# Optimization experiments

Hardware: AMD Instinct MI355X
Metric: run time of the kernel (lower is better)

## Reference

```python
import jax, jax.numpy as jnp
import numpy as np

D = 512    # feature_dim
NH = 8     # n_head
LQ = 1024  # query length
LK = 1024  # key/value length
B = 4      # batch
TEMP = 30.0


def setup_inputs() -> dict:
    key = jax.random.key(0)
    ks = jax.random.split(key, 10)
    s = (2.0 / D) ** 0.5  # init: normal(0, sqrt(2/out_features))
    t = lambda k, shp: jax.random.normal(k, shp, dtype=jnp.float32)
    return {
        'query_real': t(ks[0], (LQ, B, D)),
        'query_imag': t(ks[1], (LQ, B, D)),
        'key_real': t(ks[2], (LK, B, D)),
        'key_imag': t(ks[3], (LK, B, D)),
        'value_real': t(ks[4], (LK, B, D)),
        'value_imag': t(ks[5], (LK, B, D)),
        # per-head stacked Linear weights [NH, out, in] (torch Linear: x @ W.T + b)
        'WK_real': t(ks[6], (NH, D, D)) * s,
        'WK_imag': t(ks[7], (NH, D, D)) * s,
        'WV_real': t(ks[8], (NH, D, D)) * s,
        'WV_imag': t(ks[9], (NH, D, D)) * s,
        'bK_real': jnp.zeros((NH, D), jnp.float32),
        'bK_imag': jnp.zeros((NH, D), jnp.float32),
        'bV_real': jnp.zeros((NH, D), jnp.float32),
        'bV_imag': jnp.zeros((NH, D), jnp.float32),
    }


def reference(query_real, query_imag, key_real, key_imag, value_real, value_imag,
              WK_real, WK_imag, WV_real, WV_imag,
              bK_real, bK_imag, bV_real, bV_imag):
    # stacked per-head linear: x [L,B,D], W [H,E,D], b [H,E] -> [H,L,B,E]
    lin = lambda x, W, b: jnp.einsum('lbd,hed->hlbe', x, W) + b[:, None, None, :]
    # complex projection of keys with WK (real/imag parts)
    kr = lin(key_real, WK_real, bK_real) - lin(key_imag, WK_imag, bK_imag)
    ki = lin(key_real, WK_imag, bK_imag) + lin(key_imag, WK_real, bK_real)
    # queries are projected with the WV weights (as in the source)
    qr = lin(query_real, WV_real, bV_real) - lin(query_imag, WV_imag, bV_imag)
    qi = lin(query_real, WV_imag, bV_imag) + lin(query_imag, WV_real, bV_real)
    # complex dot product q*k (no conjugate), magnitude -> scores [H,B,Lq,Lk]
    dr = jnp.einsum('hqbd,hpbd->hbqp', qr, kr) - jnp.einsum('hqbd,hpbd->hbqp', qi, ki)
    di = jnp.einsum('hqbd,hpbd->hbqp', qi, kr) + jnp.einsum('hqbd,hpbd->hbqp', qr, ki)
    mag = jnp.sqrt(dr * dr + di * di)
    aff = jax.nn.softmax(mag * TEMP, axis=-1)  # softmax over keys
    # weighted value sum; values are the RAW inputs (not projected)
    out_real = jnp.einsum('hbqp,pbd->qbhd', aff, value_real).reshape(LQ, B, NH * D)
    out_imag = jnp.einsum('hbqp,pbd->qbhd', aff, value_imag).reshape(LQ, B, NH * D)
    return out_real, out_imag
```

## Files before the change

kernel.cpp:

```cpp
#include <hip/hip_runtime.h>
#include <math.h>

typedef _Float16 h8_t __attribute__((ext_vector_type(8)));
typedef _Float16 h4_t __attribute__((ext_vector_type(4)));
typedef float    f4_t __attribute__((ext_vector_type(4)));

#define MFMA16(a, b, c) __builtin_amdgcn_mfma_f32_16x16x32_f16((a), (b), (c), 0, 0, 0)

typedef const __attribute__((address_space(1))) void* gas1_t;
typedef __attribute__((address_space(3))) void* las3_t;
__device__ __forceinline__ void gload16(const void* g, void* l) {
  __builtin_amdgcn_global_load_lds((gas1_t)g, (las3_t)l, 16, 0, 0);
}

constexpr int L   = 1024;
constexpr int NB  = 4;
constexpr int NHh = 8;
constexpr int D   = 512;
constexpr int M1  = L * NB;
constexpr int K1  = 2 * D;
constexpr int N1  = NHh * 2 * D;
constexpr int HB  = NHh * NB;

constexpr size_t PL_A2 = (size_t)HB * L * K1 * 2;
constexpr size_t PL_BS = (size_t)HB * 3 * L * D * 2;
constexpr size_t OFF_R0 = 0;
constexpr size_t OFF_A2 = 134217728;
constexpr size_t OFF_BS = OFF_A2 + 2 * PL_A2;
constexpr size_t OFF_VT = OFF_BS + 2 * PL_BS;
constexpr size_t WS_NEED = OFF_VT + (size_t)NB * 1024 * 1024 * 2;
constexpr size_t PL_AX = (size_t)M1 * K1 * 2;
constexpr size_t ST_AQ = 0;
constexpr size_t ST_AK = 2 * PL_AX;
constexpr size_t PL_W  = (size_t)N1 * K1 * 2;
constexpr size_t ST_WQ = 4 * PL_AX;
constexpr size_t ST_WK = ST_WQ + 2 * PL_W;

static __device__ __forceinline__ void split32(float x, _Float16& hi, _Float16& lo) {
  _Float16 h = (_Float16)x;
  hi = h;
  lo = (_Float16)(x - (float)h);
}


__global__ void k_stage_x(const float* __restrict__ qre, const float* __restrict__ qim,
                          const float* __restrict__ kre, const float* __restrict__ kim,
                          _Float16* __restrict__ qhi, _Float16* __restrict__ qlo,
                          _Float16* __restrict__ khi, _Float16* __restrict__ klo) {
  const float* re; const float* im; _Float16* hi; _Float16* lo;
  if (blockIdx.y == 0) { re = qre; im = qim; hi = qhi; lo = qlo; }
  else                 { re = kre; im = kim; hi = khi; lo = klo; }
  int t = blockIdx.x * 256 + threadIdx.x;
  size_t idx = (size_t)t * 4;
  int m = (int)(idx >> 10), k = (int)(idx & 1023);
  const float* src = (k < 512) ? (re + (size_t)m * 512 + k) : (im + (size_t)m * 512 + (k - 512));
  f4_t v = *reinterpret_cast<const f4_t*>(src);
  h4_t h, l;
#pragma unroll
  for (int j = 0; j < 4; ++j) {
    _Float16 hh, ll; split32(v[j], hh, ll); h[j] = hh; l[j] = ll;
  }
  int sw = ((m >> 1) & 3) << 3;
  size_t dst = (size_t)m * 1024 + (k ^ sw);
  *reinterpret_cast<h4_t*>(hi + dst) = h;
  *reinterpret_cast<h4_t*>(lo + dst) = l;
}

__global__ void k_stage_w(const float* __restrict__ WVr, const float* __restrict__ WVi,
                          const float* __restrict__ WKr, const float* __restrict__ WKi,
                          _Float16* __restrict__ qhi, _Float16* __restrict__ qlo,
                          _Float16* __restrict__ khi, _Float16* __restrict__ klo) {
  const float* Wr; const float* Wi; _Float16* hi; _Float16* lo;
  if (blockIdx.y == 0) { Wr = WVr; Wi = WVi; hi = qhi; lo = qlo; }
  else                 { Wr = WKr; Wi = WKi; hi = khi; lo = klo; }
  int t = blockIdx.x * 256 + threadIdx.x;
  size_t idx = (size_t)t * 4;
  int n = (int)(idx >> 10), k = (int)(idx & 1023);
  int h = n >> 10, ri = (n >> 9) & 1, e = n & 511;
  size_t rowoff = ((size_t)(h * 512 + e)) * 512;
  const float* src; float sgn = 1.0f;
  if (ri == 0) {
    if (k < 512) src = Wr + rowoff + k;
    else { src = Wi + rowoff + (k - 512); sgn = -1.0f; }
  } else {
    if (k < 512) src = Wi + rowoff + k;
    else src = Wr + rowoff + (k - 512);
  }
  f4_t v = *reinterpret_cast<const f4_t*>(src);
  h4_t h4, l4;
#pragma unroll
  for (int j = 0; j < 4; ++j) {
    _Float16 hh, ll; split32(sgn * v[j], hh, ll); h4[j] = hh; l4[j] = ll;
  }
  int sw = ((n >> 1) & 3) << 3;
  size_t dst = (size_t)n * 1024 + (k ^ sw);
  *reinterpret_cast<h4_t*>(hi + dst) = h4;
  *reinterpret_cast<h4_t*>(lo + dst) = l4;
}

__global__ void k_stage_v(const float* __restrict__ vr, const float* __restrict__ vi,
                          _Float16* __restrict__ vt) {
  __shared__ float tile[64][65];
  int pt = blockIdx.x, nt = blockIdx.y, b = blockIdx.z;
  const float* src = (nt < 8) ? vr : vi;
  int dbase = (nt & 7) * 64;
  for (int i = threadIdx.x; i < 4096; i += 256) {
    int pl = i >> 6, dl = i & 63;
    tile[pl][dl] = src[((size_t)(pt * 64 + pl) * 4 + b) * 512 + dbase + dl];
  }
  __syncthreads();
  for (int i = threadIdx.x; i < 4096; i += 256) {
    int nl = i >> 6, pl = i & 63;
    int psw = pl ^ ((nl & 7) << 3);
    vt[((size_t)b * 1024 + nt * 64 + nl) * 1024 + pt * 64 + psw] = (_Float16)tile[pl][nl];
  }
}

__global__ __launch_bounds__(512, 1) void k_proj(
    const _Float16* __restrict__ Ahi, const _Float16* __restrict__ Alo,
    const _Float16* __restrict__ Bhi, const _Float16* __restrict__ Blo,
    const float* __restrict__ biasR, const float* __restrict__ biasI,
    _Float16* __restrict__ OutHi, _Float16* __restrict__ OutLo, int mode) {
  extern __shared__ __align__(16) _Float16 dldsP[];
  const int tid = threadIdx.x;
  const int id = blockIdx.x;
  const int xcd = id & 7, j = id >> 3;
  const int cm = j >> 2, cn = j & 3;
  const int m0 = cm * 256;
  const int n0 = (xcd * 4 + cn) * 256;
  const int wid = tid >> 6, lane = tid & 63;
  const int wm = (wid >> 1) * 64, wn = (wid & 1) * 128;
  const int fr = lane & 15, fq = lane >> 4;
  const int csw = (fq ^ ((fr >> 1) & 3)) * 8;

  const int srow = tid >> 2, sslot = tid & 3;
  const int soff = srow * 32 + sslot * 8;
  const _Float16* gA0 = Ahi + (size_t)(m0 + srow) * 1024 + sslot * 8;
  const _Float16* gA1 = gA0 + 128 * 1024;
  const _Float16* gA2 = Alo + (size_t)(m0 + srow) * 1024 + sslot * 8;
  const _Float16* gA3 = gA2 + 128 * 1024;
  const _Float16* gB0 = Bhi + (size_t)(n0 + srow) * 1024 + sslot * 8;
  const _Float16* gB1 = gB0 + 128 * 1024;
  const _Float16* gB2 = Blo + (size_t)(n0 + srow) * 1024 + sslot * 8;
  const _Float16* gB3 = gB2 + 128 * 1024;

  auto STAGE_A = [&](int buf) {
    _Float16* Lb = dldsP + buf * 32768;
    gload16(gA0, &Lb[soff]);
    gload16(gA1, &Lb[4096 + soff]);
    gload16(gA2, &Lb[8192 + soff]);
    gload16(gA3, &Lb[12288 + soff]);
    gA0 += 32; gA1 += 32; gA2 += 32; gA3 += 32;
  };
  auto STAGE_B = [&](int buf) {
    _Float16* Lb = dldsP + buf * 32768;
    gload16(gB0, &Lb[16384 + soff]);
    gload16(gB1, &Lb[20480 + soff]);
    gload16(gB2, &Lb[24576 + soff]);
    gload16(gB3, &Lb[28672 + soff]);
    gB0 += 32; gB1 += 32; gB2 += 32; gB3 += 32;
  };

  f4_t acc[4][8] = {};

  STAGE_A(0); STAGE_B(0);
  asm volatile("s_waitcnt vmcnt(0)" ::: "memory");
  __builtin_amdgcn_s_barrier();

  for (int kt = 0; kt < 32; ++kt) {
    const int cur = kt & 1, nxt = cur ^ 1;
    const _Float16* Lb = dldsP + cur * 32768;
    h8_t af[4][2];
#pragma unroll
    for (int mi = 0; mi < 4; ++mi) {
      int r = wm + mi * 16 + fr;
      af[mi][0] = *reinterpret_cast<const h8_t*>(&Lb[r * 32 + csw]);
      af[mi][1] = *reinterpret_cast<const h8_t*>(&Lb[8192 + r * 32 + csw]);
    }
    h8_t bh[4], bl[4];
#pragma unroll
    for (int ni = 0; ni < 4; ++ni) {
      int rn = wn + ni * 16 + fr;
      bh[ni] = *reinterpret_cast<const h8_t*>(&Lb[16384 + rn * 32 + csw]);
      bl[ni] = *reinterpret_cast<const h8_t*>(&Lb[24576 + rn * 32 + csw]);
    }
    if (kt < 31) STAGE_A(nxt);
    __builtin_amdgcn_s_barrier();
    __builtin_amdgcn_s_setprio(1);
#pragma unroll
    for (int ni = 0; ni < 4; ++ni)
#pragma unroll
      for (int mi = 0; mi < 4; ++mi) {
        acc[mi][ni] = MFMA16(af[mi][0], bh[ni], acc[mi][ni]);
        acc[mi][ni] = MFMA16(af[mi][0], bl[ni], acc[mi][ni]);
        acc[mi][ni] = MFMA16(af[mi][1], bh[ni], acc[mi][ni]);
      }
    __builtin_amdgcn_s_setprio(0);
    __builtin_amdgcn_s_barrier();
#pragma unroll
    for (int ni = 0; ni < 4; ++ni) {
      int rn = wn + (ni + 4) * 16 + fr;
      bh[ni] = *reinterpret_cast<const h8_t*>(&Lb[16384 + rn * 32 + csw]);
      bl[ni] = *reinterpret_cast<const h8_t*>(&Lb[24576 + rn * 32 + csw]);
    }
    if (kt < 31) STAGE_B(nxt);
    __builtin_amdgcn_s_barrier();
    __builtin_amdgcn_s_setprio(1);
#pragma unroll
    for (int ni = 0; ni < 4; ++ni)
#pragma unroll
      for (int mi = 0; mi < 4; ++mi) {
        acc[mi][ni + 4] = MFMA16(af[mi][0], bh[ni], acc[mi][ni + 4]);
        acc[mi][ni + 4] = MFMA16(af[mi][0], bl[ni], acc[mi][ni + 4]);
        acc[mi][ni + 4] = MFMA16(af[mi][1], bh[ni], acc[mi][ni + 4]);
      }
    __builtin_amdgcn_s_setprio(0);
    if (kt < 31) asm volatile("s_waitcnt vmcnt(0)" ::: "memory");
    __builtin_amdgcn_s_barrier();
  }

#pragma unroll
  for (int mi = 0; mi < 4; ++mi)
#pragma unroll
    for (int ni = 0; ni < 8; ++ni)
#pragma unroll
      for (int r = 0; r < 4; ++r) {
        int m = m0 + wm + mi * 16 + fq * 4 + r;
        int n = n0 + wn + ni * 16 + fr;
        int h = n >> 10, ri = (n >> 9) & 1, e = n & 511;
        float bias = (ri == 0) ? (biasR[h * 512 + e] - biasI[h * 512 + e])
                               : (biasI[h * 512 + e] + biasR[h * 512 + e]);
        float val = acc[mi][ni][r] + bias;
        _Float16 hi, lo; split32(val, hi, lo);
        int lb = m & 3;
        int lrow = m >> 2;
        int hb = h * 4 + lb;
        int sw = ((lrow >> 1) & 3) << 3;
        if (mode == 0) {
          size_t dst = ((size_t)hb * 1024 + lrow) * 1024 + ((ri * 512 + e) ^ sw);
          OutHi[dst] = hi; OutLo[dst] = lo;
        } else {
          int esw = e ^ sw;
          if (ri == 0) {
            size_t dst = (((size_t)hb * 3 + 0) * 1024 + lrow) * 512 + esw;
            OutHi[dst] = hi; OutLo[dst] = lo;
          } else {
            size_t d1 = (((size_t)hb * 3 + 1) * 1024 + lrow) * 512 + esw;
            size_t d2 = (((size_t)hb * 3 + 2) * 1024 + lrow) * 512 + esw;
            OutHi[d1] = hi;  OutLo[d1] = lo;
            OutHi[d2] = -hi; OutLo[d2] = -lo;
          }
        }
      }
}

__global__ __launch_bounds__(512, 1) void k_score(
    const _Float16* __restrict__ A2hi, const _Float16* __restrict__ A2lo,
    const _Float16* __restrict__ BShi, const _Float16* __restrict__ BSlo,
    float* __restrict__ mag) {
  extern __shared__ __align__(16) _Float16 dldsS[];
  const int tid = threadIdx.x;
  const int id = blockIdx.x;
  const int xcd = id & 7, j = id >> 3;
  const int hb = xcd * 4 + (j >> 5);
  const int r5 = j & 31;
  const int m0 = (r5 >> 3) * 256, n0 = (r5 & 7) * 128;
  const int wid = tid >> 6, lane = tid & 63;
  const int wm = (wid >> 1) * 64, wn = (wid & 1) * 64;
  const int fr = lane & 15, fq = lane >> 4;
  const int csw = (fq ^ ((fr >> 1) & 3)) * 8;

  const _Float16* Abh = A2hi + (size_t)hb * 1048576;
  const _Float16* Abl = A2lo + (size_t)hb * 1048576;
  const _Float16* BShb = BShi + (size_t)hb * 3 * 524288;
  const _Float16* BSlb = BSlo + (size_t)hb * 3 * 524288;

  const int srow = tid >> 2, sslot = tid & 3;
  const int soff = srow * 32 + sslot * 8;
  const size_t bbase = (size_t)(n0 + srow) * 512 + sslot * 8;
  const _Float16* gA0 = Abh + (size_t)(m0 + srow) * 1024 + sslot * 8;
  const _Float16* gA1 = gA0 + 128 * 1024;
  const _Float16* gA2 = Abl + (size_t)(m0 + srow) * 1024 + sslot * 8;
  const _Float16* gA3 = gA2 + 128 * 1024;
  const _Float16* gB0 = BShb + bbase;
  const _Float16* gB1 = BSlb + bbase;
  const _Float16* gB2 = BShb + 524288 + bbase;
  const _Float16* gB3 = BSlb + 524288 + bbase;

  auto STAGE_A = [&](int buf) {
    _Float16* Lb = dldsS + buf * 32768;
    gload16(gA0, &Lb[soff]);
    gload16(gA1, &Lb[4096 + soff]);
    gload16(gA2, &Lb[8192 + soff]);
    gload16(gA3, &Lb[12288 + soff]);
    gA0 += 32; gA1 += 32; gA2 += 32; gA3 += 32;
  };
  auto STAGE_B = [&](int buf, int kt) {
    if (kt == 16) {
      gB0 = BShb + 2 * 524288 + bbase;
      gB1 = BSlb + 2 * 524288 + bbase;
      gB2 = BShb + bbase;
      gB3 = BSlb + bbase;
    }
    _Float16* Lb = dldsS + buf * 32768;
    gload16(gB0, &Lb[16384 + soff]);
    gload16(gB1, &Lb[20480 + soff]);
    gload16(gB2, &Lb[24576 + soff]);
    gload16(gB3, &Lb[28672 + soff]);
    gB0 += 32; gB1 += 32; gB2 += 32; gB3 += 32;
  };

  f4_t adr[4][4] = {}, adi[4][4] = {};

  STAGE_A(0); STAGE_B(0, 0);
  asm volatile("s_waitcnt vmcnt(0)" ::: "memory");
  __builtin_amdgcn_s_barrier();

  for (int kt = 0; kt < 32; ++kt) {
    const int cur = kt & 1, nxt = cur ^ 1;
    const _Float16* Lb = dldsS + cur * 32768;
    h8_t af[4][2];
#pragma unroll
    for (int mi = 0; mi < 4; ++mi) {
      int r = wm + mi * 16 + fr;
      af[mi][0] = *reinterpret_cast<const h8_t*>(&Lb[r * 32 + csw]);
      af[mi][1] = *reinterpret_cast<const h8_t*>(&Lb[8192 + r * 32 + csw]);
    }
    h8_t drh[2], drl[2], dih[2], dil[2];
#pragma unroll
    for (int ni = 0; ni < 2; ++ni) {
      int rn = wn + ni * 16 + fr;
      drh[ni] = *reinterpret_cast<const h8_t*>(&Lb[16384 + rn * 32 + csw]);
      drl[ni] = *reinterpret_cast<const h8_t*>(&Lb[20480 + rn * 32 + csw]);
      dih[ni] = *reinterpret_cast<const h8_t*>(&Lb[24576 + rn * 32 + csw]);
      dil[ni] = *reinterpret_cast<const h8_t*>(&Lb[28672 + rn * 32 + csw]);
    }
    if (kt < 31) STAGE_A(nxt);
    __builtin_amdgcn_s_barrier();
    __builtin_amdgcn_s_setprio(1);
#pragma unroll
    for (int ni = 0; ni < 2; ++ni)
#pragma unroll
      for (int mi = 0; mi < 4; ++mi) {
        adr[mi][ni] = MFMA16(af[mi][0], drh[ni], adr[mi][ni]);
        adr[mi][ni] = MFMA16(af[mi][0], drl[ni], adr[mi][ni]);
        adr[mi][ni] = MFMA16(af[mi][1], drh[ni], adr[mi][ni]);
        adi[mi][ni] = MFMA16(af[mi][0], dih[ni], adi[mi][ni]);
        adi[mi][ni] = MFMA16(af[mi][0], dil[ni], adi[mi][ni]);
        adi[mi][ni] = MFMA16(af[mi][1], dih[ni], adi[mi][ni]);
      }
    __builtin_amdgcn_s_setprio(0);
    __builtin_amdgcn_s_barrier();
#pragma unroll
    for (int ni = 0; ni < 2; ++ni) {
      int rn = wn + (ni + 2) * 16 + fr;
      drh[ni] = *reinterpret_cast<const h8_t*>(&Lb[16384 + rn * 32 + csw]);
      drl[ni] = *reinterpret_cast<const h8_t*>(&Lb[20480 + rn * 32 + csw]);
      dih[ni] = *reinterpret_cast<const h8_t*>(&Lb[24576 + rn * 32 + csw]);
      dil[ni] = *reinterpret_cast<const h8_t*>(&Lb[28672 + rn * 32 + csw]);
    }
    if (kt < 31) STAGE_B(nxt, kt + 1);
    __builtin_amdgcn_s_barrier();
    __builtin_amdgcn_s_setprio(1);
#pragma unroll
    for (int ni = 0; ni < 2; ++ni)
#pragma unroll
      for (int mi = 0; mi < 4; ++mi) {
        adr[mi][ni + 2] = MFMA16(af[mi][0], drh[ni], adr[mi][ni + 2]);
        adr[mi][ni + 2] = MFMA16(af[mi][0], drl[ni], adr[mi][ni + 2]);
        adr[mi][ni + 2] = MFMA16(af[mi][1], drh[ni], adr[mi][ni + 2]);
        adi[mi][ni + 2] = MFMA16(af[mi][0], dih[ni], adi[mi][ni + 2]);
        adi[mi][ni + 2] = MFMA16(af[mi][0], dil[ni], adi[mi][ni + 2]);
        adi[mi][ni + 2] = MFMA16(af[mi][1], dih[ni], adi[mi][ni + 2]);
      }
    __builtin_amdgcn_s_setprio(0);
    if (kt < 31) asm volatile("s_waitcnt vmcnt(0)" ::: "memory");
    __builtin_amdgcn_s_barrier();
  }

  float* mb = mag + (size_t)hb * 1048576;
#pragma unroll
  for (int mi = 0; mi < 4; ++mi)
#pragma unroll
    for (int ni = 0; ni < 4; ++ni)
#pragma unroll
      for (int r = 0; r < 4; ++r) {
        int q = m0 + wm + mi * 16 + fq * 4 + r;
        int p = n0 + wn + ni * 16 + fr;
        float dr = adr[mi][ni][r], di = adi[mi][ni][r];
        mb[(size_t)q * 1024 + p] = sqrtf(dr * dr + di * di) * 30.0f;
      }
}

__global__ void k_softmax(const float* __restrict__ mag, _Float16* __restrict__ aff) {
  const size_t base = (size_t)blockIdx.x * 1024;
  const int q = blockIdx.x & 1023;
  const int sw = (q & 7) << 3;
  const int tid = threadIdx.x;
  const int wid = tid >> 6, lane = tid & 63;
  float v[4];
#pragma unroll
  for (int j = 0; j < 4; ++j) v[j] = mag[base + tid + j * 256];
  float mx = fmaxf(fmaxf(v[0], v[1]), fmaxf(v[2], v[3]));
#pragma unroll
  for (int o = 32; o > 0; o >>= 1) mx = fmaxf(mx, __shfl_xor(mx, o));
  __shared__ float red[8];
  if (lane == 0) red[wid] = mx;
  __syncthreads();
  mx = fmaxf(fmaxf(red[0], red[1]), fmaxf(red[2], red[3]));
  float e[4]; float s = 0.0f;
#pragma unroll
  for (int j = 0; j < 4; ++j) { e[j] = __expf(v[j] - mx); s += e[j]; }
#pragma unroll
  for (int o = 32; o > 0; o >>= 1) s += __shfl_xor(s, o);
  if (lane == 0) red[4 + wid] = s;
  __syncthreads();
  s = red[4] + red[5] + red[6] + red[7];
  float inv = 1.0f / s;
#pragma unroll
  for (int j = 0; j < 4; ++j) aff[base + j * 256 + (tid ^ sw)] = (_Float16)(e[j] * inv);
}

__global__ __launch_bounds__(256, 2) void k_pv(
    const _Float16* __restrict__ aff, const _Float16* __restrict__ vt,
    float* __restrict__ out) {
  extern __shared__ __align__(16) _Float16 dldsV[];
  const int tid = threadIdx.x;
  const int id = blockIdx.x;
  const int xcd = id & 7, j = id >> 3;
  const int b = xcd >> 1;
  const int h = (xcd & 1) * 4 + (j >> 6);
  const int hb = h * 4 + b;
  const int r6 = j & 63;
  const int m0 = (r6 >> 3) * 128, n0 = (r6 & 7) * 128;
  const int wid = tid >> 6, lane = tid & 63;
  const int wm = (wid >> 1) * 64, wn = (wid & 1) * 64;
  const int fr = lane & 15, fq = lane >> 4;
  const int s7 = fr & 7;

  const _Float16* Ab = aff + (size_t)hb * 1048576;
  const _Float16* Bb = vt + (size_t)b * 1048576;

  const int srow = tid >> 3, sslot = tid & 7;
  const int soff = srow * 64 + sslot * 8;
  const _Float16* gA = Ab + (size_t)(m0 + srow) * 1024 + sslot * 8;
  const _Float16* gB = Bb + (size_t)(n0 + srow) * 1024 + sslot * 8;

  auto STAGE = [&](int buf) {
    _Float16* Lb = dldsV + buf * 16384;
    gload16(gA,             &Lb[soff]);
    gload16(gA + 32 * 1024, &Lb[2048 + soff]);
    gload16(gA + 64 * 1024, &Lb[4096 + soff]);
    gload16(gA + 96 * 1024, &Lb[6144 + soff]);
    gload16(gB,             &Lb[8192 + soff]);
    gload16(gB + 32 * 1024, &Lb[10240 + soff]);
    gload16(gB + 64 * 1024, &Lb[12288 + soff]);
    gload16(gB + 96 * 1024, &Lb[14336 + soff]);
    gA += 64; gB += 64;
  };

  f4_t acc[4][4] = {};
  auto compute = [&](int buf) {
    const _Float16* Lb = dldsV + buf * 16384;
#pragma unroll
    for (int k32 = 0; k32 < 2; ++k32) {
      const int csw = ((k32 * 4 + fq) ^ s7) * 8;
      h8_t af[4];
#pragma unroll
      for (int mi = 0; mi < 4; ++mi)
        af[mi] = *reinterpret_cast<const h8_t*>(&Lb[(wm + mi * 16 + fr) * 64 + csw]);
#pragma unroll
      for (int ni = 0; ni < 4; ++ni) {
        h8_t bf = *reinterpret_cast<const h8_t*>(&Lb[8192 + (wn + ni * 16 + fr) * 64 + csw]);
#pragma unroll
        for (int mi = 0; mi < 4; ++mi) acc[mi][ni] = MFMA16(af[mi], bf, acc[mi][ni]);
      }
    }
  };

  STAGE(0);
  for (int kt = 0; kt < 15; ++kt) {
    __builtin_amdgcn_s_barrier();
    STAGE((kt + 1) & 1);
    asm volatile("s_waitcnt vmcnt(8)" ::: "memory");
    __builtin_amdgcn_s_barrier();
    compute(kt & 1);
  }
  __builtin_amdgcn_s_barrier();
  asm volatile("s_waitcnt vmcnt(0)" ::: "memory");
  __builtin_amdgcn_s_barrier();
  compute(1);

#pragma unroll
  for (int mi = 0; mi < 4; ++mi)
#pragma unroll
    for (int ni = 0; ni < 4; ++ni)
#pragma unroll
      for (int r = 0; r < 4; ++r) {
        int q = m0 + wm + mi * 16 + fq * 4 + r;
        int n = n0 + wn + ni * 16 + fr;
        int d = n & 511;
        size_t o = (size_t)(n < 512 ? 0 : 16777216) + (((size_t)q * 4 + b) * 8 + h) * 512 + d;
        out[o] = acc[mi][ni][r];
      }
}

extern "C" void kernel_launch(void* const* d_in, const int* in_sizes, int n_in,
                              void* d_out, int out_size, void* d_ws, size_t ws_size,
                              hipStream_t stream) {
  (void)in_sizes; (void)n_in; (void)out_size;
  if (ws_size < WS_NEED) return;

  hipFuncSetAttribute((const void*)k_score, hipFuncAttributeMaxDynamicSharedMemorySize, 131072);
  hipFuncSetAttribute((const void*)k_proj,  hipFuncAttributeMaxDynamicSharedMemorySize, 131072);
  hipFuncSetAttribute((const void*)k_pv,    hipFuncAttributeMaxDynamicSharedMemorySize, 65536);

  const float* qre = (const float*)d_in[0];
  const float* qim = (const float*)d_in[1];
  const float* kre = (const float*)d_in[2];
  const float* kim = (const float*)d_in[3];
  const float* vre = (const float*)d_in[4];
  const float* vim = (const float*)d_in[5];
  const float* WKr = (const float*)d_in[6];
  const float* WKi = (const float*)d_in[7];
  const float* WVr = (const float*)d_in[8];
  const float* WVi = (const float*)d_in[9];
  const float* bKr = (const float*)d_in[10];
  const float* bKi = (const float*)d_in[11];
  const float* bVr = (const float*)d_in[12];
  const float* bVi = (const float*)d_in[13];

  char* ws = (char*)d_ws;
  _Float16* AqHi = (_Float16*)(ws + ST_AQ);
  _Float16* AqLo = (_Float16*)(ws + ST_AQ + PL_AX);
  _Float16* AkHi = (_Float16*)(ws + ST_AK);
  _Float16* AkLo = (_Float16*)(ws + ST_AK + PL_AX);
  _Float16* WqHi = (_Float16*)(ws + ST_WQ);
  _Float16* WqLo = (_Float16*)(ws + ST_WQ + PL_W);
  _Float16* WkHi = (_Float16*)(ws + ST_WK);
  _Float16* WkLo = (_Float16*)(ws + ST_WK + PL_W);
  _Float16* A2Hi = (_Float16*)(ws + OFF_A2);
  _Float16* A2Lo = (_Float16*)(ws + OFF_A2 + PL_A2);
  _Float16* BSHi = (_Float16*)(ws + OFF_BS);
  _Float16* BSLo = (_Float16*)(ws + OFF_BS + PL_BS);
  _Float16* Vt   = (_Float16*)(ws + OFF_VT);
  float*    magp = (float*)(ws + OFF_R0);
  _Float16* affp = (_Float16*)(ws + OFF_A2);
  float*    outp = (float*)d_out;

  k_stage_x<<<dim3(4096, 2), dim3(256), 0, stream>>>(qre, qim, kre, kim, AqHi, AqLo, AkHi, AkLo);
  k_stage_w<<<dim3(8192, 2), dim3(256), 0, stream>>>(WVr, WVi, WKr, WKi, WqHi, WqLo, WkHi, WkLo);
  k_stage_v<<<dim3(16, 16, 4), dim3(256), 0, stream>>>(vre, vim, Vt);
  k_proj<<<dim3(512), dim3(512), 131072, stream>>>(AqHi, AqLo, WqHi, WqLo, bVr, bVi, A2Hi, A2Lo, 0);
  k_proj<<<dim3(512), dim3(512), 131072, stream>>>(AkHi, AkLo, WkHi, WkLo, bKr, bKi, BSHi, BSLo, 1);
  k_score<<<dim3(1024), dim3(512), 131072, stream>>>(A2Hi, A2Lo, BSHi, BSLo, magp);
  k_softmax<<<dim3(32 * 1024), dim3(256), 0, stream>>>(magp, affp);
  k_pv<<<dim3(2048), dim3(256), 65536, stream>>>(affp, Vt, outp);
}
```

Measured before the change: 907.8 us.

## Software-pipeline LDS fragment reads across k-steps in projection and score GEMMs

Restructures the main loops of both split-fp16 GEMM kernels so that next-tile LDS fragment reads (A and first B half) are issued ahead of the MFMA blocks of the current tile, merging A and B global-to-LDS staging into one issue. Barriers drop from four to two per k-step and sched_barrier fences keep the compiler from reordering MFMAs around the reads. This is meant to hide LDS read latency behind MFMAs and cut sync overhead, at the cost of extra fragment registers, which may lower occupancy.

```diff
diff --git a/kernel.cpp b/kernel.cpp
--- a/kernel.cpp
+++ b/kernel.cpp
@@ -6,6 +6,7 @@
 typedef float    f4_t __attribute__((ext_vector_type(4)));
 
 #define MFMA16(a, b, c) __builtin_amdgcn_mfma_f32_16x16x32_f16((a), (b), (c), 0, 0, 0)
+#define SCHEDB() __builtin_amdgcn_sched_barrier(0)
 
 typedef const __attribute__((address_space(1))) void* gas1_t;
 typedef __attribute__((address_space(3))) void* las3_t;
@@ -144,48 +145,60 @@
   const _Float16* gB2 = Blo + (size_t)(n0 + srow) * 1024 + sslot * 8;
   const _Float16* gB3 = gB2 + 128 * 1024;
 
-  auto STAGE_A = [&](int buf) {
+  auto STAGE = [&](int buf) {
     _Float16* Lb = dldsP + buf * 32768;
     gload16(gA0, &Lb[soff]);
     gload16(gA1, &Lb[4096 + soff]);
     gload16(gA2, &Lb[8192 + soff]);
     gload16(gA3, &Lb[12288 + soff]);
-    gA0 += 32; gA1 += 32; gA2 += 32; gA3 += 32;
-  };
-  auto STAGE_B = [&](int buf) {
-    _Float16* Lb = dldsP + buf * 32768;
     gload16(gB0, &Lb[16384 + soff]);
     gload16(gB1, &Lb[20480 + soff]);
     gload16(gB2, &Lb[24576 + soff]);
     gload16(gB3, &Lb[28672 + soff]);
+    gA0 += 32; gA1 += 32; gA2 += 32; gA3 += 32;
     gB0 += 32; gB1 += 32; gB2 += 32; gB3 += 32;
   };
 
   f4_t acc[4][8] = {};
-
-  STAGE_A(0); STAGE_B(0);
-  asm volatile("s_waitcnt vmcnt(0)" ::: "memory");
-  __builtin_amdgcn_s_barrier();
-
-  for (int kt = 0; kt < 32; ++kt) {
-    const int cur = kt & 1, nxt = cur ^ 1;
-    const _Float16* Lb = dldsP + cur * 32768;
-    h8_t af[4][2];
+  h8_t af[4][2], bh[4], bl[4], bh2[4], bl2[4];
+
+  auto READ_AF = [&](const _Float16* Lb) {
 #pragma unroll
     for (int mi = 0; mi < 4; ++mi) {
       int r = wm + mi * 16 + fr;
       af[mi][0] = *reinterpret_cast<const h8_t*>(&Lb[r * 32 + csw]);
       af[mi][1] = *reinterpret_cast<const h8_t*>(&Lb[8192 + r * 32 + csw]);
     }
-    h8_t bh[4], bl[4];
+  };
+  auto READ_B0 = [&](const _Float16* Lb) {
 #pragma unroll
     for (int ni = 0; ni < 4; ++ni) {
       int rn = wn + ni * 16 + fr;
       bh[ni] = *reinterpret_cast<const h8_t*>(&Lb[16384 + rn * 32 + csw]);
       bl[ni] = *reinterpret_cast<const h8_t*>(&Lb[24576 + rn * 32 + csw]);
     }
-    if (kt < 31) STAGE_A(nxt);
-    __builtin_amdgcn_s_barrier();
+  };
+  auto READ_B1 = [&](const _Float16* Lb) {
+#pragma unroll
+    for (int ni = 0; ni < 4; ++ni) {
+      int rn = wn + (ni + 4) * 16 + fr;
+      bh2[ni] = *reinterpret_cast<const h8_t*>(&Lb[16384 + rn * 32 + csw]);
+      bl2[ni] = *reinterpret_cast<const h8_t*>(&Lb[24576 + rn * 32 + csw]);
+    }
+  };
+
+  STAGE(0);
+  asm volatile("s_waitcnt vmcnt(0)" ::: "memory");
+  __builtin_amdgcn_s_barrier();
+  READ_AF(dldsP); READ_B0(dldsP);
+
+  for (int kt = 0; kt < 32; ++kt) {
+    const int cur = kt & 1, nxt = cur ^ 1;
+    const _Float16* Lc = dldsP + cur * 32768;
+    const _Float16* Ln = dldsP + nxt * 32768;
+    READ_B1(Lc);
+    if (kt < 31) STAGE(nxt);
+    SCHEDB();
     __builtin_amdgcn_s_setprio(1);
 #pragma unroll
     for (int ni = 0; ni < 4; ++ni)
@@ -196,26 +209,22 @@
         acc[mi][ni] = MFMA16(af[mi][1], bh[ni], acc[mi][ni]);
       }
     __builtin_amdgcn_s_setprio(0);
+    if (kt < 31) asm volatile("s_waitcnt vmcnt(0)" ::: "memory");
     __builtin_amdgcn_s_barrier();
-#pragma unroll
-    for (int ni = 0; ni < 4; ++ni) {
-      int rn = wn + (ni + 4) * 16 + fr;
-      bh[ni] = *reinterpret_cast<const h8_t*>(&Lb[16384 + rn * 32 + csw]);
-      bl[ni] = *reinterpret_cast<const h8_t*>(&Lb[24576 + rn * 32 + csw]);
-    }
-    if (kt < 31) STAGE_B(nxt);
-    __builtin_amdgcn_s_barrier();
+    if (kt < 31) READ_B0(Ln);
+    SCHEDB();
     __builtin_amdgcn_s_setprio(1);
 #pragma unroll
     for (int ni = 0; ni < 4; ++ni)
 #pragma unroll
       for (int mi = 0; mi < 4; ++mi) {
-        acc[mi][ni + 4] = MFMA16(af[mi][0], bh[ni], acc[mi][ni + 4]);
-        acc[mi][ni + 4] = MFMA16(af[mi][0], bl[ni], acc[mi][ni + 4]);
-        acc[mi][ni + 4] = MFMA16(af[mi][1], bh[ni], acc[mi][ni + 4]);
+        acc[mi][ni + 4] = MFMA16(af[mi][0], bh2[ni], acc[mi][ni + 4]);
+        acc[mi][ni + 4] = MFMA16(af[mi][0], bl2[ni], acc[mi][ni + 4]);
+        acc[mi][ni + 4] = MFMA16(af[mi][1], bh2[ni], acc[mi][ni + 4]);
       }
     __builtin_amdgcn_s_setprio(0);
-    if (kt < 31) asm volatile("s_waitcnt vmcnt(0)" ::: "memory");
+    SCHEDB();
+    if (kt < 31) READ_AF(Ln);
     __builtin_amdgcn_s_barrier();
   }
 
@@ -287,46 +296,40 @@
   const _Float16* gB2 = BShb + 524288 + bbase;
   const _Float16* gB3 = BSlb + 524288 + bbase;
 
-  auto STAGE_A = [&](int buf) {
+  auto STAGE = [&](int buf, int ktn) {
+    if (ktn == 16) {
+      gB0 = BShb + 2 * 524288 + bbase;
+      gB1 = BSlb + 2 * 524288 + bbase;
+      gB2 = BShb + bbase;
+      gB3 = BSlb + bbase;
+    }
     _Float16* Lb = dldsS + buf * 32768;
     gload16(gA0, &Lb[soff]);
     gload16(gA1, &Lb[4096 + soff]);
     gload16(gA2, &Lb[8192 + soff]);
     gload16(gA3, &Lb[12288 + soff]);
-    gA0 += 32; gA1 += 32; gA2 += 32; gA3 += 32;
-  };
-  auto STAGE_B = [&](int buf, int kt) {
-    if (kt == 16) {
-      gB0 = BShb + 2 * 524288 + bbase;
-      gB1 = BSlb + 2 * 524288 + bbase;
-      gB2 = BShb + bbase;
-      gB3 = BSlb + bbase;
-    }
-    _Float16* Lb = dldsS + buf * 32768;
     gload16(gB0, &Lb[16384 + soff]);
     gload16(gB1, &Lb[20480 + soff]);
     gload16(gB2, &Lb[24576 + soff]);
     gload16(gB3, &Lb[28672 + soff]);
+    gA0 += 32; gA1 += 32; gA2 += 32; gA3 += 32;
     gB0 += 32; gB1 += 32; gB2 += 32; gB3 += 32;
   };
 
   f4_t adr[4][4] = {}, adi[4][4] = {};
-
-  STAGE_A(0); STAGE_B(0, 0);
-  asm volatile("s_waitcnt vmcnt(0)" ::: "memory");
-  __builtin_amdgcn_s_barrier();
-
-  for (int kt = 0; kt < 32; ++kt) {
-    const int cur = kt & 1, nxt = cur ^ 1;
-    const _Float16* Lb = dldsS + cur * 32768;
-    h8_t af[4][2];
+  h8_t af[4][2];
+  h8_t drh[2], drl[2], dih[2], dil[2];
+  h8_t drh2[2], drl2[2], dih2[2], dil2[2];
+
+  auto READ_AF = [&](const _Float16* Lb) {
 #pragma unroll
     for (int mi = 0; mi < 4; ++mi) {
       int r = wm + mi * 16 + fr;
       af[mi][0] = *reinterpret_cast<const h8_t*>(&Lb[r * 32 + csw]);
       af[mi][1] = *reinterpret_cast<const h8_t*>(&Lb[8192 + r * 32 + csw]);
     }
-    h8_t drh[2], drl[2], dih[2], dil[2];
+  };
+  auto READ_B0 = [&](const _Float16* Lb) {
 #pragma unroll
     for (int ni = 0; ni < 2; ++ni) {
       int rn = wn + ni * 16 + fr;
@@ -335,8 +338,30 @@
       dih[ni] = *reinterpret_cast<const h8_t*>(&Lb[24576 + rn * 32 + csw]);
       dil[ni] = *reinterpret_cast<const h8_t*>(&Lb[28672 + rn * 32 + csw]);
     }
-    if (kt < 31) STAGE_A(nxt);
-    __builtin_amdgcn_s_barrier();
+  };
+  auto READ_B1 = [&](const _Float16* Lb) {
+#pragma unroll
+    for (int ni = 0; ni < 2; ++ni) {
+      int rn = wn + (ni + 2) * 16 + fr;
+      drh2[ni] = *reinterpret_cast<const h8_t*>(&Lb[16384 + rn * 32 + csw]);
+      drl2[ni] = *reinterpret_cast<const h8_t*>(&Lb[20480 + rn * 32 + csw]);
+      dih2[ni] = *reinterpret_cast<const h8_t*>(&Lb[24576 + rn * 32 + csw]);
+      dil2[ni] = *reinterpret_cast<const h8_t*>(&Lb[28672 + rn * 32 + csw]);
+    }
+  };
+
+  STAGE(0, 0);
+  asm volatile("s_waitcnt vmcnt(0)" ::: "memory");
+  __builtin_amdgcn_s_barrier();
+  READ_AF(dldsS); READ_B0(dldsS);
+
+  for (int kt = 0; kt < 32; ++kt) {
+    const int cur = kt & 1, nxt = cur ^ 1;
+    const _Float16* Lc = dldsS + cur * 32768;
+    const _Float16* Ln = dldsS + nxt * 32768;
+    READ_B1(Lc);
+    if (kt < 31) STAGE(nxt, kt + 1);
+    SCHEDB();
     __builtin_amdgcn_s_setprio(1);
 #pragma unroll
     for (int ni = 0; ni < 2; ++ni)
@@ -350,31 +375,25 @@
         adi[mi][ni] = MFMA16(af[mi][1], dih[ni], adi[mi][ni]);
       }
     __builtin_amdgcn_s_setprio(0);
+    if (kt < 31) asm volatile("s_waitcnt vmcnt(0)" ::: "memory");
     __builtin_amdgcn_s_barrier();
-#pragma unroll
-    for (int ni = 0; ni < 2; ++ni) {
-      int rn = wn + (ni + 2) * 16 + fr;
-      drh[ni] = *reinterpret_cast<const h8_t*>(&Lb[16384 + rn * 32 + csw]);
-      drl[ni] = *reinterpret_cast<const h8_t*>(&Lb[20480 + rn * 32 + csw]);
-      dih[ni] = *reinterpret_cast<const h8_t*>(&Lb[24576 + rn * 32 + csw]);
-      dil[ni] = *reinterpret_cast<const h8_t*>(&Lb[28672 + rn * 32 + csw]);
-    }
-    if (kt < 31) STAGE_B(nxt, kt + 1);
-    __builtin_amdgcn_s_barrier();
+    if (kt < 31) READ_B0(Ln);
+    SCHEDB();
     __builtin_amdgcn_s_setprio(1);
 #pragma unroll
     for (int ni = 0; ni < 2; ++ni)
 #pragma unroll
       for (int mi = 0; mi < 4; ++mi) {
-        adr[mi][ni + 2] = MFMA16(af[mi][0], drh[ni], adr[mi][ni + 2]);
-        adr[mi][ni + 2] = MFMA16(af[mi][0], drl[ni], adr[mi][ni + 2]);
-        adr[mi][ni + 2] = MFMA16(af[mi][1], drh[ni], adr[mi][ni + 2]);
-        adi[mi][ni + 2] = MFMA16(af[mi][0], dih[ni], adi[mi][ni + 2]);
-        adi[mi][ni + 2] = MFMA16(af[mi][0], dil[ni], adi[mi][ni + 2]);
-        adi[mi][ni + 2] = MFMA16(af[mi][1], dih[ni], adi[mi][ni + 2]);
+        adr[mi][ni + 2] = MFMA16(af[mi][0], drh2[ni], adr[mi][ni + 2]);
+        adr[mi][ni + 2] = MFMA16(af[mi][0], drl2[ni], adr[mi][ni + 2]);
+        adr[mi][ni + 2] = MFMA16(af[mi][1], drh2[ni], adr[mi][ni + 2]);
+        adi[mi][ni + 2] = MFMA16(af[mi][0], dih2[ni], adi[mi][ni + 2]);
+        adi[mi][ni + 2] = MFMA16(af[mi][0], dil2[ni], adi[mi][ni + 2]);
+        adi[mi][ni + 2] = MFMA16(af[mi][1], dih2[ni], adi[mi][ni + 2]);
       }
     __builtin_amdgcn_s_setprio(0);
-    if (kt < 31) asm volatile("s_waitcnt vmcnt(0)" ::: "memory");
+    SCHEDB();
+    if (kt < 31) READ_AF(Ln);
     __builtin_amdgcn_s_barrier();
   }
 
```

Result: slower. 943.6 us (+3.9%).

## Triple-buffer A tiles and deepen prefetch in projection and score GEMMs

Applied to the files above, without the earlier changes.

Restructures the LDS pipeline in k_proj and k_score. A tiles now use a three-slot ring and are prefetched two k-steps ahead, while B tiles stay double-buffered. The end-of-iteration full vmcnt(0) wait is replaced by a partial vmcnt(4) wait at the top of each iteration, so one stage of loads can stay in flight across the barrier. This hides more global-load latency but raises dynamic LDS per block to 160 KB.

```diff
diff --git a/kernel.cpp b/kernel.cpp
--- a/kernel.cpp
+++ b/kernel.cpp
@@ -144,47 +144,54 @@
   const _Float16* gB2 = Blo + (size_t)(n0 + srow) * 1024 + sslot * 8;
   const _Float16* gB3 = gB2 + 128 * 1024;
 
-  auto STAGE_A = [&](int buf) {
-    _Float16* Lb = dldsP + buf * 32768;
+  auto STAGE_A = [&](int slot) {
+    _Float16* Lb = dldsP + slot * 16384;
     gload16(gA0, &Lb[soff]);
     gload16(gA1, &Lb[4096 + soff]);
     gload16(gA2, &Lb[8192 + soff]);
     gload16(gA3, &Lb[12288 + soff]);
     gA0 += 32; gA1 += 32; gA2 += 32; gA3 += 32;
   };
-  auto STAGE_B = [&](int buf) {
-    _Float16* Lb = dldsP + buf * 32768;
-    gload16(gB0, &Lb[16384 + soff]);
-    gload16(gB1, &Lb[20480 + soff]);
-    gload16(gB2, &Lb[24576 + soff]);
-    gload16(gB3, &Lb[28672 + soff]);
+  auto STAGE_B = [&](int slot) {
+    _Float16* Lb = dldsP + 49152 + slot * 16384;
+    gload16(gB0, &Lb[soff]);
+    gload16(gB1, &Lb[4096 + soff]);
+    gload16(gB2, &Lb[8192 + soff]);
+    gload16(gB3, &Lb[12288 + soff]);
     gB0 += 32; gB1 += 32; gB2 += 32; gB3 += 32;
   };
 
   f4_t acc[4][8] = {};
 
-  STAGE_A(0); STAGE_B(0);
-  asm volatile("s_waitcnt vmcnt(0)" ::: "memory");
-  __builtin_amdgcn_s_barrier();
-
+  STAGE_A(0);
+  STAGE_B(0);
+  STAGE_A(1);
+
+  int sA = 0;
   for (int kt = 0; kt < 32; ++kt) {
-    const int cur = kt & 1, nxt = cur ^ 1;
-    const _Float16* Lb = dldsP + cur * 32768;
+    const int sB = kt & 1;
+    const _Float16* LA = dldsP + sA * 16384;
+    const _Float16* LB = dldsP + 49152 + sB * 16384;
+    if (kt < 31) asm volatile("s_waitcnt vmcnt(4)" ::: "memory");
+    else         asm volatile("s_waitcnt vmcnt(0)" ::: "memory");
+    __builtin_amdgcn_s_barrier();
     h8_t af[4][2];
 #pragma unroll
     for (int mi = 0; mi < 4; ++mi) {
       int r = wm + mi * 16 + fr;
-      af[mi][0] = *reinterpret_cast<const h8_t*>(&Lb[r * 32 + csw]);
-      af[mi][1] = *reinterpret_cast<const h8_t*>(&Lb[8192 + r * 32 + csw]);
+      af[mi][0] = *reinterpret_cast<const h8_t*>(&LA[r * 32 + csw]);
+      af[mi][1] = *reinterpret_cast<const h8_t*>(&LA[8192 + r * 32 + csw]);
     }
     h8_t bh[4], bl[4];
 #pragma unroll
     for (int ni = 0; ni < 4; ++ni) {
       int rn = wn + ni * 16 + fr;
-      bh[ni] = *reinterpret_cast<const h8_t*>(&Lb[16384 + rn * 32 + csw]);
-      bl[ni] = *reinterpret_cast<const h8_t*>(&Lb[24576 + rn * 32 + csw]);
-    }
-    if (kt < 31) STAGE_A(nxt);
+      bh[ni] = *reinterpret_cast<const h8_t*>(&LB[rn * 32 + csw]);
+      bl[ni] = *reinterpret_cast<const h8_t*>(&LB[8192 + rn * 32 + csw]);
+    }
+    if (kt < 31) STAGE_B(sB ^ 1);
+    int sA2 = sA + 2; if (sA2 >= 3) sA2 -= 3;
+    if (kt < 30) STAGE_A(sA2);
     __builtin_amdgcn_s_barrier();
     __builtin_amdgcn_s_setprio(1);
 #pragma unroll
@@ -200,10 +207,9 @@
 #pragma unroll
     for (int ni = 0; ni < 4; ++ni) {
       int rn = wn + (ni + 4) * 16 + fr;
-      bh[ni] = *reinterpret_cast<const h8_t*>(&Lb[16384 + rn * 32 + csw]);
-      bl[ni] = *reinterpret_cast<const h8_t*>(&Lb[24576 + rn * 32 + csw]);
-    }
-    if (kt < 31) STAGE_B(nxt);
+      bh[ni] = *reinterpret_cast<const h8_t*>(&LB[rn * 32 + csw]);
+      bl[ni] = *reinterpret_cast<const h8_t*>(&LB[8192 + rn * 32 + csw]);
+    }
     __builtin_amdgcn_s_barrier();
     __builtin_amdgcn_s_setprio(1);
 #pragma unroll
@@ -215,8 +221,7 @@
         acc[mi][ni + 4] = MFMA16(af[mi][1], bh[ni], acc[mi][ni + 4]);
       }
     __builtin_amdgcn_s_setprio(0);
-    if (kt < 31) asm volatile("s_waitcnt vmcnt(0)" ::: "memory");
-    __builtin_amdgcn_s_barrier();
+    sA = sA + 1; if (sA >= 3) sA -= 3;
   }
 
 #pragma unroll
@@ -287,55 +292,62 @@
   const _Float16* gB2 = BShb + 524288 + bbase;
   const _Float16* gB3 = BSlb + 524288 + bbase;
 
-  auto STAGE_A = [&](int buf) {
-    _Float16* Lb = dldsS + buf * 32768;
+  auto STAGE_A = [&](int slot) {
+    _Float16* Lb = dldsS + slot * 16384;
     gload16(gA0, &Lb[soff]);
     gload16(gA1, &Lb[4096 + soff]);
     gload16(gA2, &Lb[8192 + soff]);
     gload16(gA3, &Lb[12288 + soff]);
     gA0 += 32; gA1 += 32; gA2 += 32; gA3 += 32;
   };
-  auto STAGE_B = [&](int buf, int kt) {
-    if (kt == 16) {
+  auto STAGE_B = [&](int slot, int ktn) {
+    if (ktn == 16) {
       gB0 = BShb + 2 * 524288 + bbase;
       gB1 = BSlb + 2 * 524288 + bbase;
       gB2 = BShb + bbase;
       gB3 = BSlb + bbase;
     }
-    _Float16* Lb = dldsS + buf * 32768;
-    gload16(gB0, &Lb[16384 + soff]);
-    gload16(gB1, &Lb[20480 + soff]);
-    gload16(gB2, &Lb[24576 + soff]);
-    gload16(gB3, &Lb[28672 + soff]);
+    _Float16* Lb = dldsS + 49152 + slot * 16384;
+    gload16(gB0, &Lb[soff]);
+    gload16(gB1, &Lb[4096 + soff]);
+    gload16(gB2, &Lb[8192 + soff]);
+    gload16(gB3, &Lb[12288 + soff]);
     gB0 += 32; gB1 += 32; gB2 += 32; gB3 += 32;
   };
 
   f4_t adr[4][4] = {}, adi[4][4] = {};
 
-  STAGE_A(0); STAGE_B(0, 0);
-  asm volatile("s_waitcnt vmcnt(0)" ::: "memory");
-  __builtin_amdgcn_s_barrier();
-
+  STAGE_A(0);
+  STAGE_B(0, 0);
+  STAGE_A(1);
+
+  int sA = 0;
   for (int kt = 0; kt < 32; ++kt) {
-    const int cur = kt & 1, nxt = cur ^ 1;
-    const _Float16* Lb = dldsS + cur * 32768;
+    const int sB = kt & 1;
+    const _Float16* LA = dldsS + sA * 16384;
+    const _Float16* LB = dldsS + 49152 + sB * 16384;
+    if (kt < 31) asm volatile("s_waitcnt vmcnt(4)" ::: "memory");
+    else         asm volatile("s_waitcnt vmcnt(0)" ::: "memory");
+    __builtin_amdgcn_s_barrier();
     h8_t af[4][2];
 #pragma unroll
     for (int mi = 0; mi < 4; ++mi) {
       int r = wm + mi * 16 + fr;
-      af[mi][0] = *reinterpret_cast<const h8_t*>(&Lb[r * 32 + csw]);
-      af[mi][1] = *reinterpret_cast<const h8_t*>(&Lb[8192 + r * 32 + csw]);
+      af[mi][0] = *reinterpret_cast<const h8_t*>(&LA[r * 32 + csw]);
+      af[mi][1] = *reinterpret_cast<const h8_t*>(&LA[8192 + r * 32 + csw]);
     }
     h8_t drh[2], drl[2], dih[2], dil[2];
 #pragma unroll
     for (int ni = 0; ni < 2; ++ni) {
       int rn = wn + ni * 16 + fr;
-      drh[ni] = *reinterpret_cast<const h8_t*>(&Lb[16384 + rn * 32 + csw]);
-      drl[ni] = *reinterpret_cast<const h8_t*>(&Lb[20480 + rn * 32 + csw]);
-      dih[ni] = *reinterpret_cast<const h8_t*>(&Lb[24576 + rn * 32 + csw]);
-      dil[ni] = *reinterpret_cast<const h8_t*>(&Lb[28672 + rn * 32 + csw]);
-    }
-    if (kt < 31) STAGE_A(nxt);
+      drh[ni] = *reinterpret_cast<const h8_t*>(&LB[rn * 32 + csw]);
+      drl[ni] = *reinterpret_cast<const h8_t*>(&LB[4096 + rn * 32 + csw]);
+      dih[ni] = *reinterpret_cast<const h8_t*>(&LB[8192 + rn * 32 + csw]);
+      dil[ni] = *reinterpret_cast<const h8_t*>(&LB[12288 + rn * 32 + csw]);
+    }
+    if (kt < 31) STAGE_B(sB ^ 1, kt + 1);
+    int sA2 = sA + 2; if (sA2 >= 3) sA2 -= 3;
+    if (kt < 30) STAGE_A(sA2);
     __builtin_amdgcn_s_barrier();
     __builtin_amdgcn_s_setprio(1);
 #pragma unroll
@@ -354,12 +366,11 @@
 #pragma unroll
     for (int ni = 0; ni < 2; ++ni) {
       int rn = wn + (ni + 2) * 16 + fr;
-      drh[ni] = *reinterpret_cast<const h8_t*>(&Lb[16384 + rn * 32 + csw]);
-      drl[ni] = *reinterpret_cast<const h8_t*>(&Lb[20480 + rn * 32 + csw]);
-      dih[ni] = *reinterpret_cast<const h8_t*>(&Lb[24576 + rn * 32 + csw]);
-      dil[ni] = *reinterpret_cast<const h8_t*>(&Lb[28672 + rn * 32 + csw]);
-    }
-    if (kt < 31) STAGE_B(nxt, kt + 1);
+      drh[ni] = *reinterpret_cast<const h8_t*>(&LB[rn * 32 + csw]);
+      drl[ni] = *reinterpret_cast<const h8_t*>(&LB[4096 + rn * 32 + csw]);
+      dih[ni] = *reinterpret_cast<const h8_t*>(&LB[8192 + rn * 32 + csw]);
+      dil[ni] = *reinterpret_cast<const h8_t*>(&LB[12288 + rn * 32 + csw]);
+    }
     __builtin_amdgcn_s_barrier();
     __builtin_amdgcn_s_setprio(1);
 #pragma unroll
@@ -374,8 +385,7 @@
         adi[mi][ni + 2] = MFMA16(af[mi][1], dih[ni], adi[mi][ni + 2]);
       }
     __builtin_amdgcn_s_setprio(0);
-    if (kt < 31) asm volatile("s_waitcnt vmcnt(0)" ::: "memory");
-    __builtin_amdgcn_s_barrier();
+    sA = sA + 1; if (sA >= 3) sA -= 3;
   }
 
   float* mb = mag + (size_t)hb * 1048576;
@@ -511,8 +521,8 @@
   (void)in_sizes; (void)n_in; (void)out_size;
   if (ws_size < WS_NEED) return;
 
-  hipFuncSetAttribute((const void*)k_score, hipFuncAttributeMaxDynamicSharedMemorySize, 131072);
-  hipFuncSetAttribute((const void*)k_proj,  hipFuncAttributeMaxDynamicSharedMemorySize, 131072);
+  hipFuncSetAttribute((const void*)k_score, hipFuncAttributeMaxDynamicSharedMemorySize, 163840);
+  hipFuncSetAttribute((const void*)k_proj,  hipFuncAttributeMaxDynamicSharedMemorySize, 163840);
   hipFuncSetAttribute((const void*)k_pv,    hipFuncAttributeMaxDynamicSharedMemorySize, 65536);
 
   const float* qre = (const float*)d_in[0];
@@ -551,9 +561,9 @@
   k_stage_x<<<dim3(4096, 2), dim3(256), 0, stream>>>(qre, qim, kre, kim, AqHi, AqLo, AkHi, AkLo);
   k_stage_w<<<dim3(8192, 2), dim3(256), 0, stream>>>(WVr, WVi, WKr, WKi, WqHi, WqLo, WkHi, WkLo);
   k_stage_v<<<dim3(16, 16, 4), dim3(256), 0, stream>>>(vre, vim, Vt);
-  k_proj<<<dim3(512), dim3(512), 131072, stream>>>(AqHi, AqLo, WqHi, WqLo, bVr, bVi, A2Hi, A2Lo, 0);
-  k_proj<<<dim3(512), dim3(512), 131072, stream>>>(AkHi, AkLo, WkHi, WkLo, bKr, bKi, BSHi, BSLo, 1);
-  k_score<<<dim3(1024), dim3(512), 131072, stream>>>(A2Hi, A2Lo, BSHi, BSLo, magp);
+  k_proj<<<dim3(512), dim3(512), 163840, stream>>>(AqHi, AqLo, WqHi, WqLo, bVr, bVi, A2Hi, A2Lo, 0);
+  k_proj<<<dim3(512), dim3(512), 163840, stream>>>(AkHi, AkLo, WkHi, WkLo, bKr, bKi, BSHi, BSLo, 1);
+  k_score<<<dim3(1024), dim3(512), 163840, stream>>>(A2Hi, A2Lo, BSHi, BSLo, magp);
   k_softmax<<<dim3(32 * 1024), dim3(256), 0, stream>>>(magp, affp);
   k_pv<<<dim3(2048), dim3(256), 65536, stream>>>(affp, Vt, outp);
 }
```

Result: slower. 953.3 us (+5.0%).
